# Kernel optimization log

Measured on AMD Instinct MI355X. Metric: run time of the kernel, lower is better.

Reference implementation:

```python
import jax, jax.numpy as jnp
import numpy as np


def setup_inputs() -> dict:
    key = jax.random.key(0)
    k0, k1, k2, k3, k4 = jax.random.split(key, 5)
    n, c, s, h, w = 4, 128, 31, 32, 22
    x = jax.random.normal(k0, (n, c, s, h, w), dtype=jnp.float32)
    # 1x1 conv to a single channel == per-pixel dot over channels + scalar bias
    scale = 1.0 / np.sqrt(c).astype(np.float32)
    w1 = jax.random.normal(k1, (c,), dtype=jnp.float32) * scale
    b1 = jax.random.normal(k2, (), dtype=jnp.float32) * 0.01
    w2 = jax.random.normal(k3, (c,), dtype=jnp.float32) * scale
    b2 = jax.random.normal(k4, (), dtype=jnp.float32) * 0.01
    return {"x": x, "w1": w1, "b1": b1, "w2": w2, "b2": b2, "top_k": 16}


def reference(x, w1, b1, w2, b2, top_k):
    n, c, s, h, w = x.shape
    hw = h * w
    ns = n * (s - 1)
    # adjacent-frame pairs; 1x1 conv (C->1) as channel contraction
    X0 = jnp.einsum('ncshw,c->nshw', x[:, :, : s - 1], w1) + b1  # (n, s-1, h, w)
    X1 = jnp.einsum('ncshw,c->nshw', x[:, :, 1:], w2) + b2       # (n, s-1, h, w)
    X0 = X0.reshape(ns, hw)
    X1 = X1.reshape(ns, hw)
    # outer-product scores per frame pair, softmax over last dim
    attention = jax.nn.softmax(X0[:, :, None] * X1[:, None, :], axis=2)  # (ns, hw, hw)
    # top-k values along last dim -> (ns, hw, k); torch .view(ns, k, h, w)
    # is a raw row-major reinterpretation, so a plain reshape is faithful.
    vals, _ = jax.lax.top_k(attention, top_k)
    vals = vals.reshape(n, s - 1, top_k, h, w)
    # trans_out: (n, s-1, k, h, w) -> (n, k, s-1, h, w)
    return jnp.transpose(vals, (0, 2, 1, 3, 4))
```

## Files before the change

### kernel.cpp

```cpp
#include <hip/hip_runtime.h>
#include <math.h>

#define NB   4
#define C    128
#define S    31
#define HW   704
#define T    30
#define NS   120
#define K    16
#define NFR  124

__global__ __launch_bounds__(768) void conv_select_kernel(
    const float* __restrict__ x,
    const float* __restrict__ w1, const float* __restrict__ b1p,
    const float* __restrict__ w2, const float* __restrict__ b2p,
    float* __restrict__ A, float* __restrict__ B,
    float* __restrict__ btop, float* __restrict__ bbot) {
  const int tid = threadIdx.x;
  const int wv    = __builtin_amdgcn_readfirstlane(tid) >> 6;
  const int cg    = wv / 3;
  const int local = tid - cg * 192;
  const bool act  = local < 176;
  const int f4    = act ? local : 175;
  const int fr    = blockIdx.x;
  const int sf    = fr % S;
  const int n     = fr / S;

  const float4* xp =
      (const float4*)(x + (((size_t)(n * C + cg * 32) * S + sf) * HW)) + f4;
  float4 a1 = make_float4(0.f, 0.f, 0.f, 0.f);
  float4 a2 = make_float4(0.f, 0.f, 0.f, 0.f);
#pragma unroll
  for (int c = 0; c < 32; ++c) {
    float4 xv = xp[(size_t)c * (S * HW / 4)];
    const float wa = w1[cg * 32 + c];
    const float wb = w2[cg * 32 + c];
    a1.x = fmaf(xv.x, wa, a1.x); a1.y = fmaf(xv.y, wa, a1.y);
    a1.z = fmaf(xv.z, wa, a1.z); a1.w = fmaf(xv.w, wa, a1.w);
    a2.x = fmaf(xv.x, wb, a2.x); a2.y = fmaf(xv.y, wb, a2.y);
    a2.z = fmaf(xv.z, wb, a2.z); a2.w = fmaf(xv.w, wb, a2.w);
  }

  __shared__ float4 s1[4][176];
  __shared__ float4 s2[4][176];
  if (act) {
    s1[cg][f4] = a1;
    s2[cg][f4] = a2;
  }
  __syncthreads();

  if (tid < 176) {
    float4 r1 = s1[0][tid], r2 = s2[0][tid];
#pragma unroll
    for (int u = 1; u < 4; ++u) {
      float4 t1 = s1[u][tid], t2 = s2[u][tid];
      r1.x += t1.x; r1.y += t1.y; r1.z += t1.z; r1.w += t1.w;
      r2.x += t2.x; r2.y += t2.y; r2.z += t2.z; r2.w += t2.w;
    }
    const float bb1 = b1p[0], bb2 = b2p[0];
    r1.x += bb1; r1.y += bb1; r1.z += bb1; r1.w += bb1;
    r2.x += bb2; r2.y += bb2; r2.z += bb2; r2.w += bb2;
    if (sf < T)
      ((float4*)(A + (size_t)(n * T + sf) * HW))[tid] = r1;
    if (sf >= 1)
      ((float4*)(B + (size_t)(n * T + sf - 1) * HW))[tid] = r2;
    s2[0][tid] = r2;
  }
  __syncthreads();

  if (tid < 64 && sf >= 1) {
    const int i = n * T + sf - 1;
    const float* bs = (const float*)&s2[0][0];
    float vt[11], vb[11];
#pragma unroll
    for (int j = 0; j < 11; ++j) {
      const float v = bs[j * 64 + tid];
      vt[j] = v;
      vb[j] = v;
    }
#pragma unroll 1
    for (int r = 0; r < K; ++r) {
      float lmT = vt[0], lmB = vb[0];
#pragma unroll
      for (int j = 1; j < 11; ++j) {
        lmT = fmaxf(lmT, vt[j]);
        lmB = fminf(lmB, vb[j]);
      }
      float gT = lmT, gB = lmB;
#pragma unroll
      for (int off = 1; off < 64; off <<= 1) {
        gT = fmaxf(gT, __shfl_xor(gT, off, 64));
        gB = fminf(gB, __shfl_xor(gB, off, 64));
      }
      const unsigned long long mT = __ballot(lmT == gT);
      const unsigned long long mB = __ballot(lmB == gB);
      if (tid == (int)(__ffsll(mT) - 1)) {
        bool done = false;
#pragma unroll
        for (int j = 0; j < 11; ++j) {
          const bool hit = (!done) && (vt[j] == gT);
          vt[j] = hit ? -INFINITY : vt[j];
          done  = done || hit;
        }
      }
      if (tid == (int)(__ffsll(mB) - 1)) {
        bool done = false;
#pragma unroll
        for (int j = 0; j < 11; ++j) {
          const bool hit = (!done) && (vb[j] == gB);
          vb[j] = hit ? INFINITY : vb[j];
          done  = done || hit;
        }
      }
      if (tid == 0) {
        btop[i * K + r] = gT;
        bbot[i * K + r] = gB;
      }
    }
  }
}

__global__ __launch_bounds__(256) void softmax_topk_kernel(
    const float* __restrict__ A, const float* __restrict__ B,
    const float* __restrict__ btop, const float* __restrict__ bbot,
    float* __restrict__ out) {
  const int lane = threadIdx.x & 63;
  const int wid  = blockIdx.x * 4 + (threadIdx.x >> 6);
  const int i    = wid / 176;
  const int rb   = wid % 176;

  const float st0 = btop[i * K];
  const float sb0 = bbot[i * K];
  const float L2E = 1.4426950408889634f;
  float av[4], a2[4], nm[4], part[4];
#pragma unroll
  for (int u = 0; u < 4; ++u) {
    av[u]   = A[i * HW + rb + u * 176];
    a2[u]   = av[u] * L2E;
    nm[u]   = -((av[u] >= 0.f) ? av[u] * st0 : av[u] * sb0) * L2E;
    part[u] = 0.f;
  }

  const float* __restrict__ bi = B + i * HW;
#pragma unroll
  for (int j = 0; j < 11; ++j) {
    const float bv = bi[j * 64 + lane];
#pragma unroll
    for (int u = 0; u < 4; ++u)
      part[u] += __builtin_amdgcn_exp2f(fmaf(a2[u], bv, nm[u]));
  }
#pragma unroll
  for (int off = 1; off < 64; off <<= 1) {
#pragma unroll
    for (int u = 0; u < 4; ++u)
      part[u] += __shfl_xor(part[u], off, 64);
  }

  if (lane < K) {
    const int n  = i / T;
    const int t  = i % T;
    float* obase = out + (((size_t)n * K) * T + t) * HW;
    const float tv = btop[i * K + lane];
    const float bv = bbot[i * K + lane];
#pragma unroll
    for (int u = 0; u < 4; ++u) {
      const int r = rb + u * 176;
      const float sel = (av[u] >= 0.f) ? tv : bv;
      const float val = __builtin_amdgcn_exp2f(fmaf(a2[u], sel, nm[u])) / part[u];
      obase[(size_t)(r / 44) * (T * HW) + (r % 44) * K + lane] = val;
    }
  }
}

extern "C" void kernel_launch(void* const* d_in, const int* in_sizes, int n_in,
                              void* d_out, int out_size, void* d_ws, size_t ws_size,
                              hipStream_t stream) {
  (void)in_sizes; (void)n_in; (void)out_size; (void)ws_size;
  const float* x  = (const float*)d_in[0];
  const float* w1 = (const float*)d_in[1];
  const float* b1 = (const float*)d_in[2];
  const float* w2 = (const float*)d_in[3];
  const float* b2 = (const float*)d_in[4];
  float* out = (float*)d_out;

  float* A    = (float*)d_ws;
  float* B    = A + NS * HW;
  float* btop = B + NS * HW;
  float* bbot = btop + NS * K;

  conv_select_kernel<<<NFR, 768, 0, stream>>>(x, w1, b1, w2, b2,
                                              A, B, btop, bbot);
  softmax_topk_kernel<<<5280, 256, 0, stream>>>(A, B, btop, bbot, out);
}
```

Baseline: 114.9 us.

## Remap softmax kernel to one row per lane with LDS-staged B

Reorganizes the softmax/top-k kernel so each lane owns one attention row, with B staged once per block in shared memory and the four waves splitting the column range and reducing partial sums through LDS. This replaces per-row cross-lane shuffle reductions and scattered 16-lane stores with a shared-memory reduction and contiguous float4 output writes. The trade-off is fewer blocks, and only one wave is active during the output phase.

```diff
diff --git a/kernel.cpp b/kernel.cpp
--- a/kernel.cpp
+++ b/kernel.cpp
@@ -124,51 +124,59 @@
     const float* __restrict__ A, const float* __restrict__ B,
     const float* __restrict__ btop, const float* __restrict__ bbot,
     float* __restrict__ out) {
-  const int lane = threadIdx.x & 63;
-  const int wid  = blockIdx.x * 4 + (threadIdx.x >> 6);
-  const int i    = wid / 176;
-  const int rb   = wid % 176;
-
+  __shared__ float4 bs4[176];
+  __shared__ float  partial[4][64];
+  __shared__ float  seltop[K], selbot[K];
+  const int tid  = threadIdx.x;
+  const int lane = tid & 63;
+  const int w    = tid >> 6;
+  const int i    = blockIdx.x / 11;
+  const int slab = blockIdx.x % 11;
+  const int n    = i / T;
+  const int tp   = i % T;
+
+  if (tid < 176) bs4[tid] = ((const float4*)(B + i * HW))[tid];
+  if (tid >= 176 && tid < 176 + K) {
+    seltop[tid - 176] = btop[i * K + (tid - 176)];
+    selbot[tid - 176] = bbot[i * K + (tid - 176)];
+  }
+
+  const int   r   = slab * 64 + lane;
+  const float a   = A[i * HW + r];
   const float st0 = btop[i * K];
   const float sb0 = bbot[i * K];
   const float L2E = 1.4426950408889634f;
-  float av[4], a2[4], nm[4], part[4];
-#pragma unroll
-  for (int u = 0; u < 4; ++u) {
-    av[u]   = A[i * HW + rb + u * 176];
-    a2[u]   = av[u] * L2E;
-    nm[u]   = -((av[u] >= 0.f) ? av[u] * st0 : av[u] * sb0) * L2E;
-    part[u] = 0.f;
-  }
-
-  const float* __restrict__ bi = B + i * HW;
-#pragma unroll
-  for (int j = 0; j < 11; ++j) {
-    const float bv = bi[j * 64 + lane];
-#pragma unroll
-    for (int u = 0; u < 4; ++u)
-      part[u] += __builtin_amdgcn_exp2f(fmaf(a2[u], bv, nm[u]));
-  }
-#pragma unroll
-  for (int off = 1; off < 64; off <<= 1) {
-#pragma unroll
-    for (int u = 0; u < 4; ++u)
-      part[u] += __shfl_xor(part[u], off, 64);
-  }
-
-  if (lane < K) {
-    const int n  = i / T;
-    const int t  = i % T;
-    float* obase = out + (((size_t)n * K) * T + t) * HW;
-    const float tv = btop[i * K + lane];
-    const float bv = bbot[i * K + lane];
-#pragma unroll
-    for (int u = 0; u < 4; ++u) {
-      const int r = rb + u * 176;
-      const float sel = (av[u] >= 0.f) ? tv : bv;
-      const float val = __builtin_amdgcn_exp2f(fmaf(a2[u], sel, nm[u])) / part[u];
-      obase[(size_t)(r / 44) * (T * HW) + (r % 44) * K + lane] = val;
-    }
+  const float a2  = a * L2E;
+  const float nm  = -((a >= 0.f) ? a * st0 : a * sb0) * L2E;
+  __syncthreads();
+
+  float p0 = 0.f, p1 = 0.f, p2 = 0.f, p3 = 0.f;
+#pragma unroll 11
+  for (int j = 0; j < 44; ++j) {
+    const float4 bq = bs4[w * 44 + j];
+    p0 += __builtin_amdgcn_exp2f(fmaf(a2, bq.x, nm));
+    p1 += __builtin_amdgcn_exp2f(fmaf(a2, bq.y, nm));
+    p2 += __builtin_amdgcn_exp2f(fmaf(a2, bq.z, nm));
+    p3 += __builtin_amdgcn_exp2f(fmaf(a2, bq.w, nm));
+  }
+  partial[w][lane] = (p0 + p1) + (p2 + p3);
+  __syncthreads();
+
+  if (w == 0) {
+    const float part =
+        (partial[0][lane] + partial[1][lane]) +
+        (partial[2][lane] + partial[3][lane]);
+    const float rp = 1.f / part;
+    float ov[16];
+#pragma unroll
+    for (int t = 0; t < K; ++t) {
+      const float sel = (a >= 0.f) ? seltop[t] : selbot[t];
+      ov[t] = __builtin_amdgcn_exp2f(fmaf(a2, sel, nm)) * rp;
+    }
+    float* op = out + (((size_t)(n * K + r / 44)) * T + tp) * HW + (r % 44) * K;
+#pragma unroll
+    for (int t4 = 0; t4 < 4; ++t4)
+      ((float4*)op)[t4] = ((const float4*)ov)[t4];
   }
 }
 
@@ -190,5 +198,5 @@
 
   conv_select_kernel<<<NFR, 768, 0, stream>>>(x, w1, b1, w2, b2,
                                               A, B, btop, bbot);
-  softmax_topk_kernel<<<5280, 256, 0, stream>>>(A, B, btop, bbot, out);
+  softmax_topk_kernel<<<NS * 11, 256, 0, stream>>>(A, B, btop, bbot, out);
 }
```

Result: faster. 107.9 us (-6.1%).
